# Performance work log

Hardware: AMD Instinct MI355X
Metric: run time of the kernel (lower is better)

Reference implementation:

```python
import jax, jax.numpy as jnp
import numpy as np

NUM_EXPERTS = 8
TOPK = 2


def setup_inputs() -> dict:
    key = jax.random.key(0)
    k1, k2, k3, k4 = jax.random.split(key, 4)
    T = 16384           # num_tokens * topk
    D = 2048            # intermediate_size_per_rank
    H = 4096            # hidden_dim
    intermediate_states = jax.random.normal(k1, (T, D), dtype=jnp.float32)
    w = jax.random.normal(k2, (NUM_EXPERTS, D, H), dtype=jnp.float32) * 0.02
    topk_weight = jax.random.uniform(k3, (T,), dtype=jnp.float32)
    topk_ids = jax.random.randint(k4, (T,), 0, NUM_EXPERTS, dtype=jnp.int32)
    return {"intermediate_states": intermediate_states, "w": w,
            "topk_weight": topk_weight, "topk_ids": topk_ids}


def reference(intermediate_states, w, topk_weight, topk_ids):
    # intermediate_states: [T, D] with T = num_tokens * topk
    # w: [E, D, H]; topk_ids/topk_weight: [T]
    T, D = intermediate_states.shape
    E, _, H = w.shape
    # per-expert masked matmul loop (E is small and fixed), matching the torch loop:
    # out[mask] = x[mask] @ w[i] * weight[mask]
    out = jnp.zeros((T, H), dtype=intermediate_states.dtype)
    for i in range(E):
        m = (topk_ids == i).astype(intermediate_states.dtype)[:, None]  # [T,1]
        out = out + ((intermediate_states * m) @ w[i]) * topk_weight[:, None]
    # topk-weighted sum over the topk slots per token
    output = out.reshape(T // TOPK, TOPK, H).sum(axis=1)  # [T/topk, H]
    # world_size == 1 -> reduce_scatter_tensor is the identity
    return output
```

## Files before the change

### kernel.cpp

```cpp
#include <hip/hip_runtime.h>
#include <hip/hip_bf16.h>

#define T_TOK   16384
#define DDIM    2048
#define HDIM    4096
#define NEXP    8
#define BM      256
#define BN      256
#define NKT     64
#define NKS     32
#define NBAND   (HDIM / BN)
#define MAX_TILES 72
#define KTB     16384
#define NBLK    (MAX_TILES * NBAND)
#define PW_BLOCKS 32768
#define PA_BLOCKS (MAX_TILES * NKT)

typedef __attribute__((ext_vector_type(4))) float f32x4;
typedef __attribute__((ext_vector_type(8))) __bf16 bf16x8;

#define WS_TILE_EXPERT 16
#define WS_TILE_START  (16 + MAX_TILES)
#define WS_TILE_NROWS  (16 + 2*MAX_TILES)
#define WS_ROW_IDS     1024
#define WS_SLOT_POS    18432

#define WS_APACK_OFF   131072ULL
#define WS_APACK_SZ    ((size_t)MAX_TILES * NKT * KTB)
#define WS_WB_OFF      (WS_APACK_OFF + WS_APACK_SZ)
#define WS_WB_SZ       ((size_t)NEXP * NBAND * NKT * KTB)

#define WS2_APACK_OFF  262144ULL
#define WS2_WB_OFF     (WS2_APACK_OFF + WS_APACK_SZ)
#define WS2_Y_OFF      (WS2_WB_OFF + WS_WB_SZ)
#define WS2_Y_SZ       ((size_t)T_TOK * HDIM * 2)
#define WS2_NEED       (WS2_Y_OFF + WS2_Y_SZ)


__device__ __forceinline__ void gload16(const void* g, void* l) {
    __builtin_amdgcn_global_load_lds(
        (const __attribute__((address_space(1))) void*)g,
        (__attribute__((address_space(3))) void*)l, 16, 0, 0);
}

__global__ __launch_bounds__(1024)
void routing_kernel(const int* __restrict__ topk_ids, int* __restrict__ wsi,
                    int* __restrict__ slot_pos) {
    __shared__ int cnt[NEXP];
    __shared__ int base[NEXP];
    int tid = threadIdx.x;
    if (tid < NEXP) cnt[tid] = 0;
    __syncthreads();
    for (int i = tid; i < T_TOK; i += 1024)
        atomicAdd(&cnt[topk_ids[i]], 1);
    __syncthreads();
    if (tid == 0) {
        int acc = 0, nt = 0;
        for (int e = 0; e < NEXP; ++e) {
            base[e] = acc;
            int c = cnt[e];
            for (int off = 0; off < c; off += BM) {
                wsi[WS_TILE_EXPERT + nt] = e;
                wsi[WS_TILE_START + nt]  = acc + off;
                wsi[WS_TILE_NROWS + nt]  = (c - off < BM) ? (c - off) : BM;
                nt++;
            }
            acc += c;
        }
        wsi[0] = nt;
    }
    __syncthreads();
    if (tid < NEXP) cnt[tid] = base[tid];
    __syncthreads();
    for (int i = tid; i < T_TOK; i += 1024) {
        int pos = atomicAdd(&cnt[topk_ids[i]], 1);
        wsi[WS_ROW_IDS + pos] = i;
        if (slot_pos) slot_pos[i] = pos;
    }
}

__global__ __launch_bounds__(256)
void pack_all_kernel(const float* __restrict__ W, const float* __restrict__ X,
                     const int* __restrict__ wsi,
                     unsigned char* __restrict__ wb, unsigned char* __restrict__ apack) {
    const int bid = blockIdx.x;
    if (bid < PW_BLOCKS) {
        long long u = (long long)bid * 256 + threadIdx.x;
        int n  = (int)(u % HDIM);
        int kb = (int)((u / HDIM) & 255);
        int e  = (int)(u / ((long long)HDIM * 256));
        const float* src = W + ((size_t)e * DDIM + (size_t)kb * 8) * HDIM + n;
        bf16x8 h;
        #pragma unroll
        for (int j = 0; j < 8; ++j)
            h[j] = (__bf16)src[(size_t)j * HDIM];
        int band = n >> 8;
        int row  = n & 255;
        int kt   = kb >> 2;
        int q    = kb & 3;
        unsigned char* dst = wb + (((size_t)(e * NBAND + band) * NKT + kt) * KTB) + row * 64;
        const int qsw = (row >> 1) & 3;
        *reinterpret_cast<bf16x8*>(dst + ((q ^ qsw) << 4)) = h;
    } else {
        const int pa = bid - PW_BLOCKS;
        const int tile = pa >> 6;
        const int kt   = pa & 63;
        if (tile >= wsi[0]) return;
        const int rstart = wsi[WS_TILE_START + tile];
        const int nrows  = wsi[WS_TILE_NROWS + tile];
        const int r = threadIdx.x;
        unsigned char* dst = apack + ((size_t)tile * NKT + kt) * KTB + r * 64;
        const int qsw = (r >> 1) & 3;
        bf16x8 v0, v1, v2, v3;
        if (r < nrows) {
            int slot = wsi[WS_ROW_IDS + rstart + r];
            const f32x4* p = reinterpret_cast<const f32x4*>(X + (size_t)slot * DDIM + kt * 32);
            f32x4 f[8];
            #pragma unroll
            for (int i = 0; i < 8; ++i) f[i] = p[i];
            #pragma unroll
            for (int j = 0; j < 4; ++j) { v0[j] = (__bf16)f[0][j]; v0[4+j] = (__bf16)f[1][j]; }
            #pragma unroll
            for (int j = 0; j < 4; ++j) { v1[j] = (__bf16)f[2][j]; v1[4+j] = (__bf16)f[3][j]; }
            #pragma unroll
            for (int j = 0; j < 4; ++j) { v2[j] = (__bf16)f[4][j]; v2[4+j] = (__bf16)f[5][j]; }
            #pragma unroll
            for (int j = 0; j < 4; ++j) { v3[j] = (__bf16)f[6][j]; v3[4+j] = (__bf16)f[7][j]; }
        } else {
            #pragma unroll
            for (int j = 0; j < 8; ++j) { v0[j]=(__bf16)0.f; v1[j]=(__bf16)0.f; v2[j]=(__bf16)0.f; v3[j]=(__bf16)0.f; }
        }
        *reinterpret_cast<bf16x8*>(dst + ((0 ^ qsw) << 4)) = v0;
        *reinterpret_cast<bf16x8*>(dst + ((1 ^ qsw) << 4)) = v1;
        *reinterpret_cast<bf16x8*>(dst + ((2 ^ qsw) << 4)) = v2;
        *reinterpret_cast<bf16x8*>(dst + ((3 ^ qsw) << 4)) = v3;
    }
}

#define STAGE_A(IMG, SB) do {                                                              \
    gload16(agB + (size_t)(IMG) * KTB,        smem + (SB) + ((IMG) & 1) * 16384 + ldst);          \
    gload16(agB + (size_t)(IMG) * KTB + 8192, smem + (SB) + ((IMG) & 1) * 16384 + 8192 + ldst);   \
} while (0)
#define STAGE_B(IMG, SB) do {                                                              \
    gload16(bgB + (size_t)(IMG) * KTB,        smem + (SB) + 32768 + ((IMG) & 1) * 16384 + ldst);        \
    gload16(bgB + (size_t)(IMG) * KTB + 8192, smem + (SB) + 32768 + ((IMG) & 1) * 16384 + 8192 + ldst); \
} while (0)
#define LDA(MB, IMG) do { _Pragma("unroll") for (int mf = 0; mf < 4; ++mf)                 \
    afr[mf] = *reinterpret_cast<const bf16x8*>(smem + cb + (IMG) * 16384 + abase + ((MB) + mf) * 1024); } while (0)
#define LDB(IMG) do { _Pragma("unroll") for (int nf = 0; nf < 4; ++nf)                     \
    bfr[nf] = *reinterpret_cast<const bf16x8*>(smem + cb + 32768 + (IMG) * 16384 + bbase + nf * 1024); } while (0)
#define PHASE_MFMA(MB) do {                                                                \
    __builtin_amdgcn_s_setprio(1);                                                         \
    _Pragma("unroll") for (int mf = 0; mf < 4; ++mf)                                       \
        _Pragma("unroll") for (int nf = 0; nf < 4; ++nf)                                   \
            acc[(MB) + mf][nf] = __builtin_amdgcn_mfma_f32_16x16x32_bf16(afr[mf], bfr[nf], acc[(MB) + mf][nf], 0, 0, 0); \
    __builtin_amdgcn_s_setprio(0);                                                         \
} while (0)
#define WAIT_LGKM_MFMA_FENCE() do {                                                        \
    __builtin_amdgcn_s_barrier();                                                          \
    asm volatile("s_waitcnt lgkmcnt(0)" ::: "memory");                                     \
    __builtin_amdgcn_sched_barrier(0);                                                     \
} while (0)

#define GEMM_PROLOGUE_AND_MAINLOOP                                                         \
    const int id  = blockIdx.x;                                                            \
    const int swz = (id & 7) * (NBLK / 8) + (id >> 3);                                     \
    const int tile = swz / NBAND;                                                          \
    const int band = swz % NBAND;                                                          \
    if (tile >= wsi[0]) return;                                                            \
    const int e      = wsi[WS_TILE_EXPERT + tile];                                         \
    const int rstart = wsi[WS_TILE_START + tile];                                          \
    const int nrows  = wsi[WS_TILE_NROWS + tile];                                          \
    extern __shared__ unsigned char smem[];                                                \
    const int t    = threadIdx.x;                                                          \
    const int lane = t & 63;                                                               \
    const int wid  = t >> 6;                                                               \
    const int wm   = wid >> 2;                                                             \
    const int wn   = wid & 3;                                                              \
    const int r16  = lane & 15;                                                            \
    const int c16  = lane >> 4;                                                            \
    const unsigned char* agB = apack + (size_t)tile * NKT * KTB + t * 16;                  \
    const unsigned char* bgB = wb + ((size_t)(e * NBAND + band) * NKT) * KTB + t * 16;     \
    const int ldst = wid * 1024;                                                           \
    const int qswz  = c16 ^ ((r16 >> 1) & 3);                                              \
    const int abase = (wm * 128 + r16) * 64 + (qswz << 4);                                 \
    const int bbase = (wn * 64 + r16) * 64 + (qswz << 4);                                  \
    f32x4 acc[8][4];                                                                       \
    _Pragma("unroll") for (int i = 0; i < 8; ++i)                                          \
        _Pragma("unroll") for (int j = 0; j < 4; ++j)                                      \
            acc[i][j] = (f32x4)(0.0f);                                                     \
    STAGE_A(0, 0); STAGE_B(0, 0); STAGE_A(1, 0); STAGE_B(1, 0);                            \
    asm volatile("s_waitcnt vmcnt(4)" ::: "memory");                                       \
    __builtin_amdgcn_s_barrier();                                                          \
    __builtin_amdgcn_sched_barrier(0);                                                     \
    _Pragma("unroll 1")                                                                    \
    for (int ks = 0; ks < NKS - 1; ++ks) {                                                 \
        const int cb = (ks & 1) << 16;                                                     \
        const int sb = cb ^ 65536;                                                         \
        bf16x8 afr[4], bfr[4];                                                             \
        LDA(0, 0); LDB(0);                                                                 \
        STAGE_A(2 * ks + 2, sb);                                                           \
        WAIT_LGKM_MFMA_FENCE();                                                            \
        PHASE_MFMA(0);                                                                     \
        __builtin_amdgcn_s_barrier();                                                      \
        LDA(4, 0);                                                                         \
        STAGE_B(2 * ks + 2, sb);                                                           \
        asm volatile("s_waitcnt vmcnt(4)" ::: "memory");                                   \
        WAIT_LGKM_MFMA_FENCE();                                                            \
        PHASE_MFMA(4);                                                                     \
        __builtin_amdgcn_s_barrier();                                                      \
        LDA(0, 1); LDB(1);                                                                 \
        STAGE_A(2 * ks + 3, sb);                                                           \
        WAIT_LGKM_MFMA_FENCE();                                                            \
        PHASE_MFMA(0);                                                                     \
        __builtin_amdgcn_s_barrier();                                                      \
        LDA(4, 1);                                                                         \
        STAGE_B(2 * ks + 3, sb);                                                           \
        asm volatile("s_waitcnt vmcnt(4)" ::: "memory");                                   \
        WAIT_LGKM_MFMA_FENCE();                                                            \
        PHASE_MFMA(4);                                                                     \
        __builtin_amdgcn_s_barrier();                                                      \
    }                                                                                      \
    {                                                                                      \
        const int cb = ((NKS - 1) & 1) << 16;                                              \
        bf16x8 afr[4], bfr[4];                                                             \
        LDA(0, 0); LDB(0);                                                                 \
        WAIT_LGKM_MFMA_FENCE();                                                            \
        PHASE_MFMA(0);                                                                     \
        __builtin_amdgcn_s_barrier();                                                      \
        LDA(4, 0);                                                                         \
        asm volatile("s_waitcnt vmcnt(0)" ::: "memory");                                   \
        WAIT_LGKM_MFMA_FENCE();                                                            \
        PHASE_MFMA(4);                                                                     \
        __builtin_amdgcn_s_barrier();                                                      \
        LDA(0, 1); LDB(1);                                                                 \
        WAIT_LGKM_MFMA_FENCE();                                                            \
        PHASE_MFMA(0);                                                                     \
        __builtin_amdgcn_s_barrier();                                                      \
        LDA(4, 1);                                                                         \
        asm volatile("s_waitcnt lgkmcnt(0)" ::: "memory");                                 \
        __builtin_amdgcn_sched_barrier(0);                                                 \
        PHASE_MFMA(4);                                                                     \
    }

__global__ __launch_bounds__(512, 2)
void gemm_fast2(const unsigned char* __restrict__ apack,
                const unsigned char* __restrict__ wb,
                const float* __restrict__ topk_weight,
                const int* __restrict__ wsi,
                __hip_bfloat16* __restrict__ yb) {
    GEMM_PROLOGUE_AND_MAINLOOP
    const int col0 = band * BN + wn * 64 + r16;
    #pragma unroll
    for (int mf = 0; mf < 8; ++mf) {
        const int rbase = wm * 128 + mf * 16 + c16 * 4;
        #pragma unroll
        for (int i = 0; i < 4; ++i) {
            int rl = rbase + i;
            if (rl < nrows) {
                int spos = rstart + rl;
                float wt = topk_weight[wsi[WS_ROW_IDS + spos]];
                __hip_bfloat16* yr = yb + (size_t)spos * HDIM + col0;
                #pragma unroll
                for (int nf = 0; nf < 4; ++nf)
                    yr[nf * 16] = (__hip_bfloat16)(acc[mf][nf][i] * wt);
            }
        }
    }
}

__global__ __launch_bounds__(512, 2)
void gemm_fast(const unsigned char* __restrict__ apack,
               const unsigned char* __restrict__ wb,
               const float* __restrict__ topk_weight,
               const int* __restrict__ wsi,
               float* __restrict__ Out) {
    GEMM_PROLOGUE_AND_MAINLOOP
    const int col0 = band * BN + wn * 64 + r16;
    #pragma unroll
    for (int mf = 0; mf < 8; ++mf) {
        const int rbase = wm * 128 + mf * 16 + c16 * 4;
        #pragma unroll
        for (int i = 0; i < 4; ++i) {
            int rl = rbase + i;
            if (rl < nrows) {
                int slot = wsi[WS_ROW_IDS + rstart + rl];
                float wt = topk_weight[slot];
                float* orow = Out + (size_t)(slot >> 1) * HDIM + col0;
                #pragma unroll
                for (int nf = 0; nf < 4; ++nf)
                    atomicAdd(orow + nf * 16, acc[mf][nf][i] * wt);
            }
        }
    }
}

__global__ __launch_bounds__(512)
void reduce_kernel(const __hip_bfloat16* __restrict__ yb,
                   const int* __restrict__ slot_pos,
                   float* __restrict__ Out) {
    const int tk = blockIdx.x;
    const int c  = threadIdx.x;
    const int p0 = slot_pos[2 * tk];
    const int p1 = slot_pos[2 * tk + 1];
    const bf16x8 a = *reinterpret_cast<const bf16x8*>(yb + (size_t)p0 * HDIM + c * 8);
    const bf16x8 b = *reinterpret_cast<const bf16x8*>(yb + (size_t)p1 * HDIM + c * 8);
    f32x4 o0, o1;
    #pragma unroll
    for (int j = 0; j < 4; ++j) o0[j] = (float)a[j] + (float)b[j];
    #pragma unroll
    for (int j = 0; j < 4; ++j) o1[j] = (float)a[4 + j] + (float)b[4 + j];
    float* orow = Out + (size_t)tk * HDIM + c * 8;
    *reinterpret_cast<f32x4*>(orow)     = o0;
    *reinterpret_cast<f32x4*>(orow + 4) = o1;
}

extern "C" void kernel_launch(void* const* d_in, const int* in_sizes, int n_in,
                              void* d_out, int out_size, void* d_ws, size_t ws_size,
                              hipStream_t stream) {
    const float* X   = (const float*)d_in[0];
    const float* W   = (const float*)d_in[1];
    const float* wgt = (const float*)d_in[2];
    const int*   ids = (const int*)d_in[3];
    float* Out = (float*)d_out;
    int*   wsi = (int*)d_ws;

    if (ws_size >= WS2_NEED) {
        unsigned char* apack = (unsigned char*)d_ws + WS2_APACK_OFF;
        unsigned char* wb    = (unsigned char*)d_ws + WS2_WB_OFF;
        __hip_bfloat16* yb   = (__hip_bfloat16*)((unsigned char*)d_ws + WS2_Y_OFF);
        int* slot_pos        = wsi + WS_SLOT_POS;
        routing_kernel<<<1, 1024, 0, stream>>>(ids, wsi, slot_pos);
        pack_all_kernel<<<PW_BLOCKS + PA_BLOCKS, 256, 0, stream>>>(W, X, wsi, wb, apack);
        gemm_fast2<<<NBLK, 512, 131072, stream>>>(apack, wb, wgt, wsi, yb);
        reduce_kernel<<<T_TOK / 2, 512, 0, stream>>>(yb, slot_pos, Out);
    } else {
        unsigned char* apack = (unsigned char*)d_ws + WS_APACK_OFF;
        unsigned char* wb    = (unsigned char*)d_ws + WS_WB_OFF;
        hipMemsetAsync(d_out, 0, (size_t)out_size * sizeof(float), stream);
        routing_kernel<<<1, 1024, 0, stream>>>(ids, wsi, nullptr);
        pack_all_kernel<<<PW_BLOCKS + PA_BLOCKS, 256, 0, stream>>>(W, X, wsi, wb, apack);
        gemm_fast<<<NBLK, 512, 131072, stream>>>(apack, wb, wgt, wsi, Out);
    }
}
```

Before: 514.1 us.

## Use 1024-thread GEMM blocks with 64x64 per-wave tiles

Doubles the GEMM workgroup from 8 to 16 waves, so each wave owns a 64x64 output tile instead of 128x64. This halves the accumulator registers per wave. Each thread now issues one global-to-LDS load per stage instead of two, and the main loop is simplified to two MFMA phases per k-step. The aim is more waves in flight to hide latency, at the cost of more LDS fragment reads per MFMA, fewer MFMAs between barriers, and the same 128KB LDS footprint. That footprint may still limit the kernel to one block per CU.

```diff
diff --git a/kernel.cpp b/kernel.cpp
--- a/kernel.cpp
+++ b/kernel.cpp
@@ -137,23 +137,17 @@
     }
 }
 
-#define STAGE_A(IMG, SB) do {                                                              \
-    gload16(agB + (size_t)(IMG) * KTB,        smem + (SB) + ((IMG) & 1) * 16384 + ldst);          \
-    gload16(agB + (size_t)(IMG) * KTB + 8192, smem + (SB) + ((IMG) & 1) * 16384 + 8192 + ldst);   \
-} while (0)
-#define STAGE_B(IMG, SB) do {                                                              \
-    gload16(bgB + (size_t)(IMG) * KTB,        smem + (SB) + 32768 + ((IMG) & 1) * 16384 + ldst);        \
-    gload16(bgB + (size_t)(IMG) * KTB + 8192, smem + (SB) + 32768 + ((IMG) & 1) * 16384 + 8192 + ldst); \
-} while (0)
-#define LDA(MB, IMG) do { _Pragma("unroll") for (int mf = 0; mf < 4; ++mf)                 \
-    afr[mf] = *reinterpret_cast<const bf16x8*>(smem + cb + (IMG) * 16384 + abase + ((MB) + mf) * 1024); } while (0)
-#define LDB(IMG) do { _Pragma("unroll") for (int nf = 0; nf < 4; ++nf)                     \
+#define STAGE_A1(IMG, SB) gload16(agB + (size_t)(IMG) * KTB, smem + (SB) + ((IMG) & 1) * 16384 + ldst)
+#define STAGE_B1(IMG, SB) gload16(bgB + (size_t)(IMG) * KTB, smem + (SB) + 32768 + ((IMG) & 1) * 16384 + ldst)
+#define LDA1(IMG) do { _Pragma("unroll") for (int mf = 0; mf < 4; ++mf)                    \
+    afr[mf] = *reinterpret_cast<const bf16x8*>(smem + cb + (IMG) * 16384 + abase + mf * 1024); } while (0)
+#define LDB1(IMG) do { _Pragma("unroll") for (int nf = 0; nf < 4; ++nf)                    \
     bfr[nf] = *reinterpret_cast<const bf16x8*>(smem + cb + 32768 + (IMG) * 16384 + bbase + nf * 1024); } while (0)
-#define PHASE_MFMA(MB) do {                                                                \
+#define PHASE_MFMA1() do {                                                                 \
     __builtin_amdgcn_s_setprio(1);                                                         \
     _Pragma("unroll") for (int mf = 0; mf < 4; ++mf)                                       \
         _Pragma("unroll") for (int nf = 0; nf < 4; ++nf)                                   \
-            acc[(MB) + mf][nf] = __builtin_amdgcn_mfma_f32_16x16x32_bf16(afr[mf], bfr[nf], acc[(MB) + mf][nf], 0, 0, 0); \
+            acc[mf][nf] = __builtin_amdgcn_mfma_f32_16x16x32_bf16(afr[mf], bfr[nf], acc[mf][nf], 0, 0, 0); \
     __builtin_amdgcn_s_setprio(0);                                                         \
 } while (0)
 #define WAIT_LGKM_MFMA_FENCE() do {                                                        \
@@ -174,23 +168,23 @@
     extern __shared__ unsigned char smem[];                                                \
     const int t    = threadIdx.x;                                                          \
     const int lane = t & 63;                                                               \
-    const int wid  = t >> 6;                                                               \
-    const int wm   = wid >> 2;                                                             \
-    const int wn   = wid & 3;                                                              \
+    const int wid  = t >> 6;                                                    \
+    const int wm   = wid >> 2;                                     \
+    const int wn   = wid & 3;                                      \
     const int r16  = lane & 15;                                                            \
     const int c16  = lane >> 4;                                                            \
     const unsigned char* agB = apack + (size_t)tile * NKT * KTB + t * 16;                  \
     const unsigned char* bgB = wb + ((size_t)(e * NBAND + band) * NKT) * KTB + t * 16;     \
     const int ldst = wid * 1024;                                                           \
     const int qswz  = c16 ^ ((r16 >> 1) & 3);                                              \
-    const int abase = (wm * 128 + r16) * 64 + (qswz << 4);                                 \
+    const int abase = (wm * 64 + r16) * 64 + (qswz << 4);                                  \
     const int bbase = (wn * 64 + r16) * 64 + (qswz << 4);                                  \
-    f32x4 acc[8][4];                                                                       \
-    _Pragma("unroll") for (int i = 0; i < 8; ++i)                                          \
+    f32x4 acc[4][4];                                                                       \
+    _Pragma("unroll") for (int i = 0; i < 4; ++i)                                          \
         _Pragma("unroll") for (int j = 0; j < 4; ++j)                                      \
             acc[i][j] = (f32x4)(0.0f);                                                     \
-    STAGE_A(0, 0); STAGE_B(0, 0); STAGE_A(1, 0); STAGE_B(1, 0);                            \
-    asm volatile("s_waitcnt vmcnt(4)" ::: "memory");                                       \
+    STAGE_A1(0, 0); STAGE_B1(0, 0); STAGE_A1(1, 0); STAGE_B1(1, 0);                        \
+    asm volatile("s_waitcnt vmcnt(2)" ::: "memory");  \
     __builtin_amdgcn_s_barrier();                                                          \
     __builtin_amdgcn_sched_barrier(0);                                                     \
     _Pragma("unroll 1")                                                                    \
@@ -198,52 +192,36 @@
         const int cb = (ks & 1) << 16;                                                     \
         const int sb = cb ^ 65536;                                                         \
         bf16x8 afr[4], bfr[4];                                                             \
-        LDA(0, 0); LDB(0);                                                                 \
-        STAGE_A(2 * ks + 2, sb);                                                           \
+                                                                         \
+        LDA1(0); LDB1(0);                                                                  \
+        STAGE_A1(2 * ks + 2, sb); STAGE_B1(2 * ks + 2, sb);                                \
+        asm volatile("s_waitcnt vmcnt(2)" ::: "memory");       \
         WAIT_LGKM_MFMA_FENCE();                                                            \
-        PHASE_MFMA(0);                                                                     \
+        PHASE_MFMA1();                                                                     \
         __builtin_amdgcn_s_barrier();                                                      \
-        LDA(4, 0);                                                                         \
-        STAGE_B(2 * ks + 2, sb);                                                           \
-        asm volatile("s_waitcnt vmcnt(4)" ::: "memory");                                   \
+                                                                          \
+        LDA1(1); LDB1(1);                                                                  \
+        STAGE_A1(2 * ks + 3, sb); STAGE_B1(2 * ks + 3, sb);                                \
+        asm volatile("s_waitcnt vmcnt(2)" ::: "memory");        \
         WAIT_LGKM_MFMA_FENCE();                                                            \
-        PHASE_MFMA(4);                                                                     \
-        __builtin_amdgcn_s_barrier();                                                      \
-        LDA(0, 1); LDB(1);                                                                 \
-        STAGE_A(2 * ks + 3, sb);                                                           \
-        WAIT_LGKM_MFMA_FENCE();                                                            \
-        PHASE_MFMA(0);                                                                     \
-        __builtin_amdgcn_s_barrier();                                                      \
-        LDA(4, 1);                                                                         \
-        STAGE_B(2 * ks + 3, sb);                                                           \
-        asm volatile("s_waitcnt vmcnt(4)" ::: "memory");                                   \
-        WAIT_LGKM_MFMA_FENCE();                                                            \
-        PHASE_MFMA(4);                                                                     \
+        PHASE_MFMA1();                                                                     \
         __builtin_amdgcn_s_barrier();                                                      \
     }                                                                                      \
-    {                                                                                      \
+    {                                                         \
         const int cb = ((NKS - 1) & 1) << 16;                                              \
         bf16x8 afr[4], bfr[4];                                                             \
-        LDA(0, 0); LDB(0);                                                                 \
+        LDA1(0); LDB1(0);                                                                  \
+        asm volatile("s_waitcnt vmcnt(0)" ::: "memory");               \
         WAIT_LGKM_MFMA_FENCE();                                                            \
-        PHASE_MFMA(0);                                                                     \
+        PHASE_MFMA1();                                                                     \
         __builtin_amdgcn_s_barrier();                                                      \
-        LDA(4, 0);                                                                         \
-        asm volatile("s_waitcnt vmcnt(0)" ::: "memory");                                   \
-        WAIT_LGKM_MFMA_FENCE();                                                            \
-        PHASE_MFMA(4);                                                                     \
-        __builtin_amdgcn_s_barrier();                                                      \
-        LDA(0, 1); LDB(1);                                                                 \
-        WAIT_LGKM_MFMA_FENCE();                                                            \
-        PHASE_MFMA(0);                                                                     \
-        __builtin_amdgcn_s_barrier();                                                      \
-        LDA(4, 1);                                                                         \
+        LDA1(1); LDB1(1);                                                                  \
         asm volatile("s_waitcnt lgkmcnt(0)" ::: "memory");                                 \
         __builtin_amdgcn_sched_barrier(0);                                                 \
-        PHASE_MFMA(4);                                                                     \
-    }
-
-__global__ __launch_bounds__(512, 2)
+        PHASE_MFMA1();                                                                     \
+    }
+
+__global__ __launch_bounds__(1024, 4)
 void gemm_fast2(const unsigned char* __restrict__ apack,
                 const unsigned char* __restrict__ wb,
                 const float* __restrict__ topk_weight,
@@ -252,8 +230,8 @@
     GEMM_PROLOGUE_AND_MAINLOOP
     const int col0 = band * BN + wn * 64 + r16;
     #pragma unroll
-    for (int mf = 0; mf < 8; ++mf) {
-        const int rbase = wm * 128 + mf * 16 + c16 * 4;
+    for (int mf = 0; mf < 4; ++mf) {
+        const int rbase = wm * 64 + mf * 16 + c16 * 4;
         #pragma unroll
         for (int i = 0; i < 4; ++i) {
             int rl = rbase + i;
@@ -269,7 +247,7 @@
     }
 }
 
-__global__ __launch_bounds__(512, 2)
+__global__ __launch_bounds__(1024, 4)
 void gemm_fast(const unsigned char* __restrict__ apack,
                const unsigned char* __restrict__ wb,
                const float* __restrict__ topk_weight,
@@ -278,8 +256,8 @@
     GEMM_PROLOGUE_AND_MAINLOOP
     const int col0 = band * BN + wn * 64 + r16;
     #pragma unroll
-    for (int mf = 0; mf < 8; ++mf) {
-        const int rbase = wm * 128 + mf * 16 + c16 * 4;
+    for (int mf = 0; mf < 4; ++mf) {
+        const int rbase = wm * 64 + mf * 16 + c16 * 4;
         #pragma unroll
         for (int i = 0; i < 4; ++i) {
             int rl = rbase + i;
@@ -332,7 +310,7 @@
         int* slot_pos        = wsi + WS_SLOT_POS;
         routing_kernel<<<1, 1024, 0, stream>>>(ids, wsi, slot_pos);
         pack_all_kernel<<<PW_BLOCKS + PA_BLOCKS, 256, 0, stream>>>(W, X, wsi, wb, apack);
-        gemm_fast2<<<NBLK, 512, 131072, stream>>>(apack, wb, wgt, wsi, yb);
+        gemm_fast2<<<NBLK, 1024, 131072, stream>>>(apack, wb, wgt, wsi, yb);
         reduce_kernel<<<T_TOK / 2, 512, 0, stream>>>(yb, slot_pos, Out);
     } else {
         unsigned char* apack = (unsigned char*)d_ws + WS_APACK_OFF;
@@ -340,6 +318,6 @@
         hipMemsetAsync(d_out, 0, (size_t)out_size * sizeof(float), stream);
         routing_kernel<<<1, 1024, 0, stream>>>(ids, wsi, nullptr);
         pack_all_kernel<<<PW_BLOCKS + PA_BLOCKS, 256, 0, stream>>>(W, X, wsi, wb, apack);
-        gemm_fast<<<NBLK, 512, 131072, stream>>>(apack, wb, wgt, wsi, Out);
-    }
-}
+        gemm_fast<<<NBLK, 1024, 131072, stream>>>(apack, wb, wgt, wsi, Out);
+    }
+}
```

New measurement: 500.8 us, median of 2. -2.6%, faster.
